# Kernel optimization log

Measured on AMD Instinct MI355X. Metric: run time of the kernel, lower is better.

## Reference

```python
import jax, jax.numpy as jnp
import numpy as np

IN_H, IN_W = 450, 450
KH, KW = 15, 15
SH, SW = 1, 1
PH, PW = 0, 0
OH = (IN_H - KH + 2 * PH) // SH + 1  # 436
OW = (IN_W - KW + 2 * PW) // SW + 1  # 436


def setup_inputs() -> dict:
    key = jax.random.key(0)
    k1, k2 = jax.random.split(key)
    x = jax.random.uniform(k1, (IN_H, IN_W), dtype=jnp.float32)
    # Untied weights: one (KH, KW) kernel per output location, matching the
    # per-column nonzeros of the original sparse weight matrix.
    W = jax.random.normal(k2, (OH, OW, KH, KW), dtype=jnp.float32)
    return {"x": x, "W": W}


def reference(x, W):
    # Equivalent to padding x, flattening, and multiplying by the huge
    # mostly-zero [(H+2p)*(W+2p), OH*OW] matrix: only the receptive-field
    # entries are nonzero, so gather patches and dot with each local kernel.
    patches = jax.lax.conv_general_dilated_patches(
        x[None, None],                 # [1, 1, IN_H, IN_W]
        filter_shape=(KH, KW),
        window_strides=(SH, SW),
        padding=[(PH, PH), (PW, PW)],
    )                                   # [1, KH*KW, OH, OW]
    out = jnp.einsum('pij,ijp->ij', patches[0], W.reshape(OH, OW, KH * KW))
    return out  # [OH, OW]
```

## Files before the change

### kernel.cpp

```cpp
#include <hip/hip_runtime.h>


constexpr int IN_W = 450;
constexpr int KH = 15, KW = 15;
constexpr int OH = 436, OW = 436;
constexpr int NOUT = OH * OW;
constexpr int KSIZE = KH * KW;

__global__ __launch_bounds__(256)
void lc2d_thread_per_out(const float* __restrict__ x,
                         const float* __restrict__ W,
                         float* __restrict__ out) {
    const int oidx = blockIdx.x * 256 + threadIdx.x;
    if (oidx >= NOUT) return;

    const int oi = oidx / OW;
    const int oj = oidx - oi * OW;

    const float* __restrict__ wp = W + (size_t)oidx * KSIZE;
    const float* __restrict__ xp = x + oi * IN_W + oj;

    float sum = 0.0f;
#pragma unroll 3
    for (int kh = 0; kh < KH; ++kh) {
        const float* __restrict__ xr = xp + kh * IN_W;
        const float* __restrict__ wr = wp + kh * KW;
#pragma unroll
        for (int kw = 0; kw < KW; ++kw) {
            sum = fmaf(wr[kw], xr[kw], sum);
        }
    }

    out[oidx] = sum;
}

extern "C" void kernel_launch(void* const* d_in, const int* in_sizes, int n_in,
                              void* d_out, int out_size, void* d_ws, size_t ws_size,
                              hipStream_t stream) {
    const float* x = (const float*)d_in[0];
    const float* W = (const float*)d_in[1];
    float* out = (float*)d_out;

    const int nblocks = (NOUT + 255) / 256;
    lc2d_thread_per_out<<<nblocks, 256, 0, stream>>>(x, W, out);
}
```

Baseline: 266.4 us.

## Map one wavefront per four outputs with coalesced float4 weight loads

Replaces the thread-per-output kernel, whose weight reads were strided by 225 floats across lanes, with one wavefront per group of four consecutive outputs. The four outputs' 900 weights are contiguous, so lanes read them as coalesced float4 loads. Each element's output and (kh,kw) offset is computed from its index, and partial sums are combined with a cross-lane shuffle reduction. The kernel is bound by weight bandwidth, so this should improve DRAM efficiency, at the cost of index arithmetic, x gathers and a shuffle reduction per wave. It also relies on OW being divisible by 4 so a quad never crosses a row.

```diff
diff --git a/kernel.cpp b/kernel.cpp
--- a/kernel.cpp
+++ b/kernel.cpp
@@ -2,36 +2,68 @@
 
 
 constexpr int IN_W = 450;
-constexpr int KH = 15, KW = 15;
-constexpr int OH = 436, OW = 436;
-constexpr int NOUT = OH * OW;
-constexpr int KSIZE = KH * KW;
+constexpr int KSIZE = 225;
+constexpr int OW = 436;
+constexpr int NOUT = 436 * 436;
+constexpr int NQUAD = NOUT / 4;
 
 __global__ __launch_bounds__(256)
-void lc2d_thread_per_out(const float* __restrict__ x,
-                         const float* __restrict__ W,
-                         float* __restrict__ out) {
-    const int oidx = blockIdx.x * 256 + threadIdx.x;
-    if (oidx >= NOUT) return;
+void lc2d_quad(const float* __restrict__ x,
+               const float* __restrict__ W,
+               float* __restrict__ out) {
+    const int lane = threadIdx.x & 63;
+    const int wave = threadIdx.x >> 6;
+    const int q = blockIdx.x * 4 + wave;
+    if (q >= NQUAD) return;
 
-    const int oi = oidx / OW;
-    const int oj = oidx - oi * OW;
+    const int o0 = q * 4;
+    const int oi = o0 / OW;
+    const int oj = o0 - oi * OW;
+    const int xb0 = oi * IN_W + oj;
 
-    const float* __restrict__ wp = W + (size_t)oidx * KSIZE;
-    const float* __restrict__ xp = x + oi * IN_W + oj;
+    const float4* __restrict__ W4 = (const float4*)W + (size_t)q * KSIZE;
+    const int el4 = lane * 4;
 
-    float sum = 0.0f;
-#pragma unroll 3
-    for (int kh = 0; kh < KH; ++kh) {
-        const float* __restrict__ xr = xp + kh * IN_W;
-        const float* __restrict__ wr = wp + kh * KW;
+    float acc[4] = {0.f, 0.f, 0.f, 0.f};
+
 #pragma unroll
-        for (int kw = 0; kw < KW; ++kw) {
-            sum = fmaf(wr[kw], xr[kw], sum);
+    for (int t = 0; t < 3; ++t) {
+        const float4 wq = W4[lane + 64 * t];
+        const float wv[4] = {wq.x, wq.y, wq.z, wq.w};
+#pragma unroll
+        for (int c = 0; c < 4; ++c) {
+            const int TH = 225 - 31 * t;
+            const bool b = (el4 + c) >= TH;
+            const unsigned k = (unsigned)(el4 + c + 31 * t - (b ? 225 : 0));
+            const int kh = (int)(k / 15u);
+            const int xi = xb0 + el4 + c + 32 * t - (b ? 224 : 0) + 435 * kh;
+            const float p = wv[c] * x[xi];
+            if (b) acc[t + 1] += p; else acc[t] += p;
+        }
+    }
+    if (el4 < 132) {
+        const float4 wq = W4[lane + 192];
+        const float wv[4] = {wq.x, wq.y, wq.z, wq.w};
+#pragma unroll
+        for (int c = 0; c < 4; ++c) {
+            const unsigned k = (unsigned)(el4 + c + 93);
+            const int kh = (int)(k / 15u);
+            const int xi = xb0 + el4 + c + 96 + 435 * kh;
+            acc[3] = fmaf(wv[c], x[xi], acc[3]);
         }
     }
 
-    out[oidx] = sum;
+#pragma unroll
+    for (int off = 32; off > 0; off >>= 1) {
+        acc[0] += __shfl_xor(acc[0], off, 64);
+        acc[1] += __shfl_xor(acc[1], off, 64);
+        acc[2] += __shfl_xor(acc[2], off, 64);
+        acc[3] += __shfl_xor(acc[3], off, 64);
+    }
+
+    if (lane == 0) {
+        ((float4*)out)[q] = make_float4(acc[0], acc[1], acc[2], acc[3]);
+    }
 }
 
 extern "C" void kernel_launch(void* const* d_in, const int* in_sizes, int n_in,
@@ -41,6 +73,6 @@
     const float* W = (const float*)d_in[1];
     float* out = (float*)d_out;
 
-    const int nblocks = (NOUT + 255) / 256;
-    lc2d_thread_per_out<<<nblocks, 256, 0, stream>>>(x, W, out);
+    const int nblocks = (NQUAD + 3) / 4;
+    lc2d_quad<<<nblocks, 256, 0, stream>>>(x, W, out);
 }
```

New measurement: 237.3 us. -11.0%, faster.

## Compute four outputs per wavefront with coalesced weight loads and LDS patch

Applied to the files above, without the earlier changes.

Reworks the mapping so each 64-lane wavefront handles four adjacent outputs. Their 900 contiguous weights are read with fully coalesced lane-strided loads, where the old code had each thread stride 225 floats through W. The shared 15x18 input patch is staged in LDS, and lanes accumulate partial sums per output, finished with cross-lane shuffle reductions. This targets the uncoalesced weight traffic that dominates a memory-bound kernel, at the cost of index arithmetic, LDS use and shuffle reductions.

```diff
diff --git a/kernel.cpp b/kernel.cpp
--- a/kernel.cpp
+++ b/kernel.cpp
@@ -2,36 +2,76 @@
 
 
 constexpr int IN_W = 450;
-constexpr int KH = 15, KW = 15;
-constexpr int OH = 436, OW = 436;
-constexpr int NOUT = OH * OW;
-constexpr int KSIZE = KH * KW;
+constexpr int OW = 436;
+constexpr int NQUAD = (436 * 436) / 4;
 
-__global__ __launch_bounds__(256)
-void lc2d_thread_per_out(const float* __restrict__ x,
-                         const float* __restrict__ W,
-                         float* __restrict__ out) {
-    const int oidx = blockIdx.x * 256 + threadIdx.x;
-    if (oidx >= NOUT) return;
+__global__ __launch_bounds__(256, 6)
+void lc2d_quad_lds(const float* __restrict__ x,
+                   const float* __restrict__ W,
+                   float* __restrict__ out) {
+    __shared__ float patch[4][270];
 
-    const int oi = oidx / OW;
-    const int oj = oidx - oi * OW;
+    const int lane = threadIdx.x & 63;
+    const int wv = threadIdx.x >> 6;
+    const int q = blockIdx.x * 4 + wv;
 
-    const float* __restrict__ wp = W + (size_t)oidx * KSIZE;
-    const float* __restrict__ xp = x + oi * IN_W + oj;
+    const int o0 = q * 4;
+    const int oi = o0 / OW;
+    const int oj = o0 - oi * OW;
+    const int xb0 = oi * IN_W + oj;
 
-    float sum = 0.0f;
-#pragma unroll 3
-    for (int kh = 0; kh < KH; ++kh) {
-        const float* __restrict__ xr = xp + kh * IN_W;
-        const float* __restrict__ wr = wp + kh * KW;
+    const float* __restrict__ Wq = W + (size_t)o0 * 225;
+
+    float wreg[14];
 #pragma unroll
-        for (int kw = 0; kw < KW; ++kw) {
-            sum = fmaf(wr[kw], xr[kw], sum);
+    for (int t = 0; t < 14; ++t) wreg[t] = Wq[lane + 64 * t];
+    float wtail = (lane < 4) ? Wq[896 + lane] : 0.0f;
+
+    float* lp = patch[wv];
+#pragma unroll
+    for (int p = 0; p < 5; ++p) {
+        const int i = lane + 64 * p;
+        if (p < 4 || i < 270) {
+            const unsigned r = (unsigned)i / 18u;
+            const int c = i - (int)r * 18;
+            lp[i] = x[xb0 + (int)r * IN_W + c];
         }
     }
+    __syncthreads();
 
-    out[oidx] = sum;
+    constexpr int S0[14] = {0,0,0,0, 1,1,1,1, 2,2,2, 3,3,3};
+    constexpr int BL[14] = {64,64,64,33, 64,64,64,2, 64,64,35, 64,64,64};
+    constexpr int K0[14] = {0,64,128,192, 31,95,159,223, 62,126,190, 29,93,157};
+
+    float acc[4] = {0.f, 0.f, 0.f, 0.f};
+#pragma unroll
+    for (int t = 0; t < 14; ++t) {
+        const bool b = (BL[t] != 64) && (lane >= BL[t]);
+        const unsigned k = (unsigned)(lane + K0[t] - (b ? 225 : 0));
+        const unsigned kh = k / 15u;
+        const int addr = (int)(k + 3u * kh) + S0[t] + (b ? 1 : 0);
+        const float pr = wreg[t] * lp[addr];
+        if (BL[t] == 64) {
+            acc[S0[t]] += pr;
+        } else {
+            if (b) acc[S0[t] + 1] += pr; else acc[S0[t]] += pr;
+        }
+    }
+    if (lane < 4) {
+        acc[3] = fmaf(wtail, lp[266 + lane], acc[3]);
+    }
+
+#pragma unroll
+    for (int a = 0; a < 4; ++a) acc[a] += __shfl_xor(acc[a], 32, 64);
+    float zA = (lane < 32) ? acc[0] : acc[1];
+    float zB = (lane < 32) ? acc[2] : acc[3];
+#pragma unroll
+    for (int off = 16; off > 0; off >>= 1) {
+        zA += __shfl_xor(zA, off, 64);
+        zB += __shfl_xor(zB, off, 64);
+    }
+    if (lane == 0)  { out[o0]     = zA; out[o0 + 2] = zB; }
+    if (lane == 32) { out[o0 + 1] = zA; out[o0 + 3] = zB; }
 }
 
 extern "C" void kernel_launch(void* const* d_in, const int* in_sizes, int n_in,
@@ -41,6 +81,6 @@
     const float* W = (const float*)d_in[1];
     float* out = (float*)d_out;
 
-    const int nblocks = (NOUT + 255) / 256;
-    lc2d_thread_per_out<<<nblocks, 256, 0, stream>>>(x, W, out);
+    const int nblocks = NQUAD / 4;
+    lc2d_quad_lds<<<nblocks, 256, 0, stream>>>(x, W, out);
 }
```

Result: faster. 234.4 us (-12.0%).
